# Optimization experiments

Measured on AMD Instinct MI355X. Metric: run time of the kernel, lower is better.

Reference implementation:

```python
import jax, jax.numpy as jnp
import numpy as np

B, D, H, O, E = 1048576, 17, 8, 6, 4  # batch, input_dim, expert_hidden, output_dim, n_clusters
G1, G2 = 64, 32  # gating hidden dims


def setup_inputs() -> dict:
    key = jax.random.key(0)
    ks = jax.random.split(key, 14)
    def w(k, shape, fan_in):
        return (jax.random.normal(k, shape, jnp.float32) / jnp.sqrt(jnp.float32(fan_in)))
    return {
        "x": jax.random.normal(ks[0], (B, D), jnp.float32),
        # per-expert MLP params, stacked on leading expert axis E
        "eW1": w(ks[1], (E, D, H), D), "eb1": w(ks[2], (E, H), D),
        "eW2": w(ks[3], (E, H, H), H), "eb2": w(ks[4], (E, H), H),
        "eW3": w(ks[5], (E, H, O), H), "eb3": w(ks[6], (E, O), H),
        # gating classifier params
        "gW1": w(ks[7], (D, G1), D), "gb1": w(ks[8], (G1,), D),
        "gW2": w(ks[9], (G1, G2), G1), "gb2": w(ks[10], (G2,), G1),
        "gW3": w(ks[11], (G2, E), G2), "gb3": w(ks[12], (E,), G2),
    }


def reference(x, eW1, eb1, eW2, eb2, eW3, eb3, gW1, gb1, gW2, gb2, gW3, gb3):
    # gating network: 17 -> 64 -> 32 -> 4 logits
    h = jax.nn.relu(x @ gW1 + gb1)
    h = jax.nn.relu(h @ gW2 + gb2)
    gating_logits = h @ gW3 + gb3  # [B, E]
    selected = jnp.argmax(gating_logits, axis=1)  # [B] hard routing
    # all experts computed (as in the original), stacked over expert axis
    e = jax.nn.relu(jnp.einsum('bi,eih->beh', x, eW1) + eb1)   # [B, E, H]
    e = jax.nn.relu(jnp.einsum('beh,ehk->bek', e, eW2) + eb2)  # [B, E, H]
    eo = jnp.einsum('bek,eko->beo', e, eW3) + eb3              # [B, E, O]
    # gather the selected expert's output per sample
    predictions = jnp.take_along_axis(eo, selected[:, None, None], axis=1)[:, 0, :]  # [B, O]
    return predictions, gating_logits
```

## Files before the change

### kernel.cpp

```cpp
#include <hip/hip_runtime.h>

#define BTOT 1048576
#define D 17
#define H 8
#define OUT 6
#define E 4
#define G1 64
#define G2 32

__global__ __launch_bounds__(256) void hybrid_ruc_kernel(
    const float* __restrict__ x,
    const float* __restrict__ eW1, const float* __restrict__ eb1,
    const float* __restrict__ eW2, const float* __restrict__ eb2,
    const float* __restrict__ eW3, const float* __restrict__ eb3,
    const float* __restrict__ gW1, const float* __restrict__ gb1,
    const float* __restrict__ gW2, const float* __restrict__ gb2,
    const float* __restrict__ gW3, const float* __restrict__ gb3,
    float* __restrict__ out)
{
    __shared__ float sx[256 * D];
    const int tid = threadIdx.x;
    const long long bbase = (long long)blockIdx.x * 256;

    #pragma unroll
    for (int k = 0; k < D; ++k) {
        int t = tid + k * 256;
        sx[t] = x[bbase * D + t];
    }
    __syncthreads();

    float xr[D];
    #pragma unroll
    for (int i = 0; i < D; ++i) xr[i] = sx[tid * D + i];

    float h2[G2];
    #pragma unroll
    for (int j = 0; j < G2; ++j) h2[j] = gb2[j];

    #pragma unroll 1
    for (int jt = 0; jt < G1 / 16; ++jt) {
        float h1t[16];
        #pragma unroll
        for (int c = 0; c < 16; ++c) h1t[c] = gb1[jt * 16 + c];
        #pragma unroll
        for (int i = 0; i < D; ++i) {
            const float xi = xr[i];
            const float* w1row = gW1 + i * G1 + jt * 16;
            #pragma unroll
            for (int c = 0; c < 16; ++c)
                h1t[c] = __builtin_fmaf(xi, w1row[c], h1t[c]);
        }
        #pragma unroll
        for (int c = 0; c < 16; ++c) {
            const float hv = fmaxf(h1t[c], 0.0f);
            const float* w2row = gW2 + (jt * 16 + c) * G2;
            #pragma unroll
            for (int j = 0; j < G2; ++j)
                h2[j] = __builtin_fmaf(hv, w2row[j], h2[j]);
        }
    }

    float lg[E];
    #pragma unroll
    for (int e = 0; e < E; ++e) lg[e] = gb3[e];
    #pragma unroll
    for (int j = 0; j < G2; ++j) {
        const float hv = fmaxf(h2[j], 0.0f);
        #pragma unroll
        for (int e = 0; e < E; ++e)
            lg[e] = __builtin_fmaf(hv, gW3[j * E + e], lg[e]);
    }

    int sel = 0;
    float best = lg[0];
    #pragma unroll
    for (int e = 1; e < E; ++e) {
        if (lg[e] > best) { best = lg[e]; sel = e; }
    }

    float pred[OUT];
    #pragma unroll
    for (int o = 0; o < OUT; ++o) pred[o] = 0.0f;

    #pragma unroll 1
    for (int e = 0; e < E; ++e) {
        float t1[H];
        #pragma unroll
        for (int h = 0; h < H; ++h) t1[h] = eb1[e * H + h];
        #pragma unroll
        for (int i = 0; i < D; ++i) {
            const float xi = xr[i];
            const float* w = eW1 + e * D * H + i * H;
            #pragma unroll
            for (int h = 0; h < H; ++h)
                t1[h] = __builtin_fmaf(xi, w[h], t1[h]);
        }
        float t2[H];
        #pragma unroll
        for (int h = 0; h < H; ++h) t2[h] = eb2[e * H + h];
        #pragma unroll
        for (int k = 0; k < H; ++k) {
            const float tv = fmaxf(t1[k], 0.0f);
            const float* w = eW2 + e * H * H + k * H;
            #pragma unroll
            for (int h = 0; h < H; ++h)
                t2[h] = __builtin_fmaf(tv, w[h], t2[h]);
        }
        float po[OUT];
        #pragma unroll
        for (int o = 0; o < OUT; ++o) po[o] = eb3[e * OUT + o];
        #pragma unroll
        for (int k = 0; k < H; ++k) {
            const float tv = fmaxf(t2[k], 0.0f);
            const float* w = eW3 + e * H * OUT + k * OUT;
            #pragma unroll
            for (int o = 0; o < OUT; ++o)
                po[o] = __builtin_fmaf(tv, w[o], po[o]);
        }
        #pragma unroll
        for (int o = 0; o < OUT; ++o)
            pred[o] = (sel == e) ? po[o] : pred[o];
    }

    const long long b = bbase + tid;
    #pragma unroll
    for (int o = 0; o < OUT; ++o) out[b * OUT + o] = pred[o];
    float* lout = out + (long long)BTOT * OUT;
    #pragma unroll
    for (int e = 0; e < E; ++e) lout[b * E + e] = lg[e];
}

extern "C" void kernel_launch(void* const* d_in, const int* in_sizes, int n_in,
                              void* d_out, int out_size, void* d_ws, size_t ws_size,
                              hipStream_t stream) {
    const float* x   = (const float*)d_in[0];
    const float* eW1 = (const float*)d_in[1];
    const float* eb1 = (const float*)d_in[2];
    const float* eW2 = (const float*)d_in[3];
    const float* eb2 = (const float*)d_in[4];
    const float* eW3 = (const float*)d_in[5];
    const float* eb3 = (const float*)d_in[6];
    const float* gW1 = (const float*)d_in[7];
    const float* gb1 = (const float*)d_in[8];
    const float* gW2 = (const float*)d_in[9];
    const float* gb2 = (const float*)d_in[10];
    const float* gW3 = (const float*)d_in[11];
    const float* gb3 = (const float*)d_in[12];
    float* out = (float*)d_out;

    dim3 grid(BTOT / 256), block(256);
    hipLaunchKernelGGL(hybrid_ruc_kernel, grid, block, 0, stream,
                       x, eW1, eb1, eW2, eb2, eW3, eb3,
                       gW1, gb1, gW2, gb2, gW3, gb3, out);
}
```

Baseline: 217.6 us.

## Use packed FP32 FMA via inline asm for gating and expert MLPs

Rewrites all the per-thread matrix-vector products with v_pk_fma_f32 inline assembly. Each instruction updates two output accumulators, with op_sel broadcasting one input element and the weight pair taken from scalar registers. This targets VALU instruction count, which dominates this compute-bound per-sample MLP. It also drops the LDS staging of x in favor of direct strided global loads, and vectorizes the output stores. The risks are less coalesced x loads, inline asm constraining the compiler's scheduling, and a possible failure to meet the "s" constraint for the weight pairs.

Result: slower. 225.2 us (+3.5%).

```diff
diff --git a/kernel.cpp b/kernel.cpp
--- a/kernel.cpp
+++ b/kernel.cpp
@@ -7,6 +7,15 @@
 #define E 4
 #define G1 64
 #define G2 32
+
+typedef float v2f __attribute__((ext_vector_type(2)));
+
+#define PKFMA_LO(acc, xp, wp)                                              \
+    asm("v_pk_fma_f32 %0, %1, %2, %0 op_sel:[0,0,0] op_sel_hi:[0,1,1]"     \
+        : "+v"(acc) : "v"(xp), "s"(wp))
+#define PKFMA_HI(acc, xp, wp)                                              \
+    asm("v_pk_fma_f32 %0, %1, %2, %0 op_sel:[1,0,0] op_sel_hi:[1,1,1]"     \
+        : "+v"(acc) : "v"(xp), "s"(wp))
 
 __global__ __launch_bounds__(256) void hybrid_ruc_kernel(
     const float* __restrict__ x,
@@ -18,59 +27,90 @@
     const float* __restrict__ gW3, const float* __restrict__ gb3,
     float* __restrict__ out)
 {
-    __shared__ float sx[256 * D];
-    const int tid = threadIdx.x;
-    const long long bbase = (long long)blockIdx.x * 256;
-
-    #pragma unroll
-    for (int k = 0; k < D; ++k) {
-        int t = tid + k * 256;
-        sx[t] = x[bbase * D + t];
-    }
-    __syncthreads();
+    const long long b = (long long)blockIdx.x * 256 + threadIdx.x;
 
     float xr[D];
     #pragma unroll
-    for (int i = 0; i < D; ++i) xr[i] = sx[tid * D + i];
-
-    float h2[G2];
-    #pragma unroll
-    for (int j = 0; j < G2; ++j) h2[j] = gb2[j];
+    for (int i = 0; i < D; ++i) xr[i] = x[b * D + i];
+    v2f xp[9];
+    #pragma unroll
+    for (int k = 0; k < 8; ++k) { xp[k].x = xr[2 * k]; xp[k].y = xr[2 * k + 1]; }
+    xp[8].x = xr[16]; xp[8].y = 0.0f;
+
+    v2f h2p[G2 / 2];
+    #pragma unroll
+    for (int j = 0; j < G2 / 2; ++j) h2p[j] = *(const v2f*)(gb2 + 2 * j);
 
     #pragma unroll 1
     for (int jt = 0; jt < G1 / 16; ++jt) {
-        float h1t[16];
-        #pragma unroll
-        for (int c = 0; c < 16; ++c) h1t[c] = gb1[jt * 16 + c];
-        #pragma unroll
-        for (int i = 0; i < D; ++i) {
-            const float xi = xr[i];
-            const float* w1row = gW1 + i * G1 + jt * 16;
-            #pragma unroll
-            for (int c = 0; c < 16; ++c)
-                h1t[c] = __builtin_fmaf(xi, w1row[c], h1t[c]);
-        }
-        #pragma unroll
-        for (int c = 0; c < 16; ++c) {
-            const float hv = fmaxf(h1t[c], 0.0f);
-            const float* w2row = gW2 + (jt * 16 + c) * G2;
-            #pragma unroll
-            for (int j = 0; j < G2; ++j)
-                h2[j] = __builtin_fmaf(hv, w2row[j], h2[j]);
-        }
-    }
-
-    float lg[E];
-    #pragma unroll
-    for (int e = 0; e < E; ++e) lg[e] = gb3[e];
-    #pragma unroll
-    for (int j = 0; j < G2; ++j) {
-        const float hv = fmaxf(h2[j], 0.0f);
-        #pragma unroll
-        for (int e = 0; e < E; ++e)
-            lg[e] = __builtin_fmaf(hv, gW3[j * E + e], lg[e]);
-    }
-
+        v2f a[8];
+        #pragma unroll
+        for (int c = 0; c < 8; ++c) a[c] = *(const v2f*)(gb1 + jt * 16 + 2 * c);
+        #pragma unroll
+        for (int k = 0; k < 8; ++k) {
+            const float* r0 = gW1 + (2 * k) * G1 + jt * 16;
+            const float* r1 = gW1 + (2 * k + 1) * G1 + jt * 16;
+            #pragma unroll
+            for (int c = 0; c < 8; ++c) {
+                v2f w = *(const v2f*)(r0 + 2 * c);
+                PKFMA_LO(a[c], xp[k], w);
+            }
+            #pragma unroll
+            for (int c = 0; c < 8; ++c) {
+                v2f w = *(const v2f*)(r1 + 2 * c);
+                PKFMA_HI(a[c], xp[k], w);
+            }
+        }
+        {
+            const float* r = gW1 + 16 * G1 + jt * 16;
+            #pragma unroll
+            for (int c = 0; c < 8; ++c) {
+                v2f w = *(const v2f*)(r + 2 * c);
+                PKFMA_LO(a[c], xp[8], w);
+            }
+        }
+        #pragma unroll
+        for (int c = 0; c < 8; ++c) {
+            a[c].x = fmaxf(a[c].x, 0.0f);
+            a[c].y = fmaxf(a[c].y, 0.0f);
+        }
+        #pragma unroll
+        for (int c = 0; c < 8; ++c) {
+            const float* r0 = gW2 + (jt * 16 + 2 * c) * G2;
+            const float* r1 = gW2 + (jt * 16 + 2 * c + 1) * G2;
+            #pragma unroll
+            for (int j = 0; j < 16; ++j) {
+                v2f w = *(const v2f*)(r0 + 2 * j);
+                PKFMA_LO(h2p[j], a[c], w);
+            }
+            #pragma unroll
+            for (int j = 0; j < 16; ++j) {
+                v2f w = *(const v2f*)(r1 + 2 * j);
+                PKFMA_HI(h2p[j], a[c], w);
+            }
+        }
+    }
+
+    v2f lgp[2];
+    lgp[0] = *(const v2f*)(gb3);
+    lgp[1] = *(const v2f*)(gb3 + 2);
+    #pragma unroll
+    for (int j2 = 0; j2 < 16; ++j2) {
+        h2p[j2].x = fmaxf(h2p[j2].x, 0.0f);
+        h2p[j2].y = fmaxf(h2p[j2].y, 0.0f);
+        const float* r0 = gW3 + (2 * j2) * E;
+        const float* r1 = gW3 + (2 * j2 + 1) * E;
+        v2f w00 = *(const v2f*)(r0);
+        v2f w01 = *(const v2f*)(r0 + 2);
+        PKFMA_LO(lgp[0], h2p[j2], w00);
+        PKFMA_LO(lgp[1], h2p[j2], w01);
+        v2f w10 = *(const v2f*)(r1);
+        v2f w11 = *(const v2f*)(r1 + 2);
+        PKFMA_HI(lgp[0], h2p[j2], w10);
+        PKFMA_HI(lgp[1], h2p[j2], w11);
+    }
+
+    float lg[E] = { lgp[0].x, lgp[0].y, lgp[1].x, lgp[1].y };
     int sel = 0;
     float best = lg[0];
     #pragma unroll
@@ -78,56 +118,96 @@
         if (lg[e] > best) { best = lg[e]; sel = e; }
     }
 
-    float pred[OUT];
-    #pragma unroll
-    for (int o = 0; o < OUT; ++o) pred[o] = 0.0f;
+    v2f predp[3];
+    #pragma unroll
+    for (int p = 0; p < 3; ++p) { predp[p].x = 0.0f; predp[p].y = 0.0f; }
 
     #pragma unroll 1
     for (int e = 0; e < E; ++e) {
-        float t1[H];
-        #pragma unroll
-        for (int h = 0; h < H; ++h) t1[h] = eb1[e * H + h];
-        #pragma unroll
-        for (int i = 0; i < D; ++i) {
-            const float xi = xr[i];
-            const float* w = eW1 + e * D * H + i * H;
-            #pragma unroll
-            for (int h = 0; h < H; ++h)
-                t1[h] = __builtin_fmaf(xi, w[h], t1[h]);
-        }
-        float t2[H];
-        #pragma unroll
-        for (int h = 0; h < H; ++h) t2[h] = eb2[e * H + h];
-        #pragma unroll
-        for (int k = 0; k < H; ++k) {
-            const float tv = fmaxf(t1[k], 0.0f);
-            const float* w = eW2 + e * H * H + k * H;
-            #pragma unroll
-            for (int h = 0; h < H; ++h)
-                t2[h] = __builtin_fmaf(tv, w[h], t2[h]);
-        }
-        float po[OUT];
-        #pragma unroll
-        for (int o = 0; o < OUT; ++o) po[o] = eb3[e * OUT + o];
-        #pragma unroll
-        for (int k = 0; k < H; ++k) {
-            const float tv = fmaxf(t2[k], 0.0f);
-            const float* w = eW3 + e * H * OUT + k * OUT;
-            #pragma unroll
-            for (int o = 0; o < OUT; ++o)
-                po[o] = __builtin_fmaf(tv, w[o], po[o]);
-        }
-        #pragma unroll
-        for (int o = 0; o < OUT; ++o)
-            pred[o] = (sel == e) ? po[o] : pred[o];
-    }
-
-    const long long b = bbase + tid;
-    #pragma unroll
-    for (int o = 0; o < OUT; ++o) out[b * OUT + o] = pred[o];
-    float* lout = out + (long long)BTOT * OUT;
-    #pragma unroll
-    for (int e = 0; e < E; ++e) lout[b * E + e] = lg[e];
+        v2f t1p[4];
+        #pragma unroll
+        for (int h = 0; h < 4; ++h) t1p[h] = *(const v2f*)(eb1 + e * H + 2 * h);
+        #pragma unroll
+        for (int k = 0; k < 8; ++k) {
+            const float* r0 = eW1 + e * D * H + (2 * k) * H;
+            const float* r1 = eW1 + e * D * H + (2 * k + 1) * H;
+            #pragma unroll
+            for (int h = 0; h < 4; ++h) {
+                v2f w = *(const v2f*)(r0 + 2 * h);
+                PKFMA_LO(t1p[h], xp[k], w);
+            }
+            #pragma unroll
+            for (int h = 0; h < 4; ++h) {
+                v2f w = *(const v2f*)(r1 + 2 * h);
+                PKFMA_HI(t1p[h], xp[k], w);
+            }
+        }
+        {
+            const float* r = eW1 + e * D * H + 16 * H;
+            #pragma unroll
+            for (int h = 0; h < 4; ++h) {
+                v2f w = *(const v2f*)(r + 2 * h);
+                PKFMA_LO(t1p[h], xp[8], w);
+            }
+        }
+        #pragma unroll
+        for (int h = 0; h < 4; ++h) {
+            t1p[h].x = fmaxf(t1p[h].x, 0.0f);
+            t1p[h].y = fmaxf(t1p[h].y, 0.0f);
+        }
+        v2f t2p[4];
+        #pragma unroll
+        for (int h = 0; h < 4; ++h) t2p[h] = *(const v2f*)(eb2 + e * H + 2 * h);
+        #pragma unroll
+        for (int k2 = 0; k2 < 4; ++k2) {
+            const float* r0 = eW2 + e * H * H + (2 * k2) * H;
+            const float* r1 = eW2 + e * H * H + (2 * k2 + 1) * H;
+            #pragma unroll
+            for (int h = 0; h < 4; ++h) {
+                v2f w = *(const v2f*)(r0 + 2 * h);
+                PKFMA_LO(t2p[h], t1p[k2], w);
+            }
+            #pragma unroll
+            for (int h = 0; h < 4; ++h) {
+                v2f w = *(const v2f*)(r1 + 2 * h);
+                PKFMA_HI(t2p[h], t1p[k2], w);
+            }
+        }
+        #pragma unroll
+        for (int h = 0; h < 4; ++h) {
+            t2p[h].x = fmaxf(t2p[h].x, 0.0f);
+            t2p[h].y = fmaxf(t2p[h].y, 0.0f);
+        }
+        v2f pop[3];
+        #pragma unroll
+        for (int p = 0; p < 3; ++p) pop[p] = *(const v2f*)(eb3 + e * OUT + 2 * p);
+        #pragma unroll
+        for (int k2 = 0; k2 < 4; ++k2) {
+            const float* r0 = eW3 + e * H * OUT + (2 * k2) * OUT;
+            const float* r1 = eW3 + e * H * OUT + (2 * k2 + 1) * OUT;
+            #pragma unroll
+            for (int p = 0; p < 3; ++p) {
+                v2f w = *(const v2f*)(r0 + 2 * p);
+                PKFMA_LO(pop[p], t2p[k2], w);
+            }
+            #pragma unroll
+            for (int p = 0; p < 3; ++p) {
+                v2f w = *(const v2f*)(r1 + 2 * p);
+                PKFMA_HI(pop[p], t2p[k2], w);
+            }
+        }
+        const bool m = (sel == e);
+        #pragma unroll
+        for (int p = 0; p < 3; ++p) predp[p] = m ? pop[p] : predp[p];
+    }
+
+    float* po = out + b * OUT;
+    *(v2f*)(po)     = predp[0];
+    *(v2f*)(po + 2) = predp[1];
+    *(v2f*)(po + 4) = predp[2];
+    float* lo = out + (long long)BTOT * OUT + b * E;
+    *(v2f*)(lo)     = lgp[0];
+    *(v2f*)(lo + 2) = lgp[1];
 }
 
 extern "C" void kernel_launch(void* const* d_in, const int* in_sizes, int n_in,
```

## Load x rows directly with vector loads, unroll loops, vectorize output stores

Applied to the files above, without the earlier changes.

Drops the shared-memory staging of x and has each thread read its own 17-float row with unaligned 4-wide vector loads, removing the barrier and LDS traffic. The gating hidden tile shrinks from 16 to 8 and both the gating and expert loops are now fully unrolled. Outputs are written with 2-wide and 4-wide vector stores. The per-thread strided x reads coalesce less well than the staged loads did, and full unrolling raises code size and register pressure.

Result: slower. 474.5 us (+118.1%).

```diff
diff --git a/kernel.cpp b/kernel.cpp
--- a/kernel.cpp
+++ b/kernel.cpp
@@ -7,6 +7,10 @@
 #define E 4
 #define G1 64
 #define G2 32
+
+typedef float v2fa __attribute__((ext_vector_type(2), aligned(8)));
+typedef float v4fa __attribute__((ext_vector_type(4), aligned(16)));
+typedef float v4fu __attribute__((ext_vector_type(4), aligned(4)));
 
 __global__ __launch_bounds__(256) void hybrid_ruc_kernel(
     const float* __restrict__ x,
@@ -18,45 +22,44 @@
     const float* __restrict__ gW3, const float* __restrict__ gb3,
     float* __restrict__ out)
 {
-    __shared__ float sx[256 * D];
-    const int tid = threadIdx.x;
-    const long long bbase = (long long)blockIdx.x * 256;
+    const long long b = (long long)blockIdx.x * 256 + threadIdx.x;
 
-    #pragma unroll
-    for (int k = 0; k < D; ++k) {
-        int t = tid + k * 256;
-        sx[t] = x[bbase * D + t];
-    }
-    __syncthreads();
-
+    const float* xrow = x + b * D;
+    v4fu xq0 = *(const v4fu*)(xrow);
+    v4fu xq1 = *(const v4fu*)(xrow + 4);
+    v4fu xq2 = *(const v4fu*)(xrow + 8);
+    v4fu xq3 = *(const v4fu*)(xrow + 12);
     float xr[D];
-    #pragma unroll
-    for (int i = 0; i < D; ++i) xr[i] = sx[tid * D + i];
+    xr[0] = xq0.x;  xr[1] = xq0.y;  xr[2] = xq0.z;  xr[3] = xq0.w;
+    xr[4] = xq1.x;  xr[5] = xq1.y;  xr[6] = xq1.z;  xr[7] = xq1.w;
+    xr[8] = xq2.x;  xr[9] = xq2.y;  xr[10] = xq2.z; xr[11] = xq2.w;
+    xr[12] = xq3.x; xr[13] = xq3.y; xr[14] = xq3.z; xr[15] = xq3.w;
+    xr[16] = xrow[16];
 
     float h2[G2];
     #pragma unroll
     for (int j = 0; j < G2; ++j) h2[j] = gb2[j];
 
-    #pragma unroll 1
-    for (int jt = 0; jt < G1 / 16; ++jt) {
-        float h1t[16];
+    #pragma unroll
+    for (int jt = 0; jt < G1 / 8; ++jt) {
+        float h1t[8];
         #pragma unroll
-        for (int c = 0; c < 16; ++c) h1t[c] = gb1[jt * 16 + c];
+        for (int c = 0; c < 8; ++c) h1t[c] = gb1[jt * 8 + c];
         #pragma unroll
         for (int i = 0; i < D; ++i) {
             const float xi = xr[i];
-            const float* w1row = gW1 + i * G1 + jt * 16;
+            const float* wr = gW1 + i * G1 + jt * 8;
             #pragma unroll
-            for (int c = 0; c < 16; ++c)
-                h1t[c] = __builtin_fmaf(xi, w1row[c], h1t[c]);
+            for (int c = 0; c < 8; ++c)
+                h1t[c] = __builtin_fmaf(xi, wr[c], h1t[c]);
         }
         #pragma unroll
-        for (int c = 0; c < 16; ++c) {
+        for (int c = 0; c < 8; ++c) {
             const float hv = fmaxf(h1t[c], 0.0f);
-            const float* w2row = gW2 + (jt * 16 + c) * G2;
+            const float* wr = gW2 + (jt * 8 + c) * G2;
             #pragma unroll
             for (int j = 0; j < G2; ++j)
-                h2[j] = __builtin_fmaf(hv, w2row[j], h2[j]);
+                h2[j] = __builtin_fmaf(hv, wr[j], h2[j]);
         }
     }
 
@@ -82,7 +85,7 @@
     #pragma unroll
     for (int o = 0; o < OUT; ++o) pred[o] = 0.0f;
 
-    #pragma unroll 1
+    #pragma unroll
     for (int e = 0; e < E; ++e) {
         float t1[H];
         #pragma unroll
@@ -90,10 +93,10 @@
         #pragma unroll
         for (int i = 0; i < D; ++i) {
             const float xi = xr[i];
-            const float* w = eW1 + e * D * H + i * H;
+            const float* wr = eW1 + e * D * H + i * H;
             #pragma unroll
             for (int h = 0; h < H; ++h)
-                t1[h] = __builtin_fmaf(xi, w[h], t1[h]);
+                t1[h] = __builtin_fmaf(xi, wr[h], t1[h]);
         }
         float t2[H];
         #pragma unroll
@@ -101,10 +104,10 @@
         #pragma unroll
         for (int k = 0; k < H; ++k) {
             const float tv = fmaxf(t1[k], 0.0f);
-            const float* w = eW2 + e * H * H + k * H;
+            const float* wr = eW2 + e * H * H + k * H;
             #pragma unroll
             for (int h = 0; h < H; ++h)
-                t2[h] = __builtin_fmaf(tv, w[h], t2[h]);
+                t2[h] = __builtin_fmaf(tv, wr[h], t2[h]);
         }
         float po[OUT];
         #pragma unroll
@@ -112,22 +115,22 @@
         #pragma unroll
         for (int k = 0; k < H; ++k) {
             const float tv = fmaxf(t2[k], 0.0f);
-            const float* w = eW3 + e * H * OUT + k * OUT;
+            const float* wr = eW3 + e * H * OUT + k * OUT;
             #pragma unroll
             for (int o = 0; o < OUT; ++o)
-                po[o] = __builtin_fmaf(tv, w[o], po[o]);
+                po[o] = __builtin_fmaf(tv, wr[o], po[o]);
         }
         #pragma unroll
         for (int o = 0; o < OUT; ++o)
             pred[o] = (sel == e) ? po[o] : pred[o];
     }
 
-    const long long b = bbase + tid;
-    #pragma unroll
-    for (int o = 0; o < OUT; ++o) out[b * OUT + o] = pred[o];
-    float* lout = out + (long long)BTOT * OUT;
-    #pragma unroll
-    for (int e = 0; e < E; ++e) lout[b * E + e] = lg[e];
+    float* po = out + b * OUT;
+    *(v2fa*)(po)     = (v2fa){pred[0], pred[1]};
+    *(v2fa*)(po + 2) = (v2fa){pred[2], pred[3]};
+    *(v2fa*)(po + 4) = (v2fa){pred[4], pred[5]};
+    float* lo = out + (long long)BTOT * OUT + b * E;
+    *(v4fa*)(lo) = (v4fa){lg[0], lg[1], lg[2], lg[3]};
 }
 
 extern "C" void kernel_launch(void* const* d_in, const int* in_sizes, int n_in,
```
